# Kernel tuning notes

Hardware: AMD Instinct MI355X
Metric: run time of the kernel (lower is better)

Reference implementation:

```python
import jax, jax.numpy as jnp
import numpy as np

B, S, E, H = 2, 2048, 1024, 16
HD = E // H


def setup_inputs() -> dict:
    key = jax.random.key(0)
    ks = jax.random.split(key, 9)
    s = 1.0 / np.sqrt(E)
    return {
        "x": jax.random.normal(ks[0], (B, S, E), dtype=jnp.float32),
        "wq": jax.random.uniform(ks[1], (E, E), jnp.float32, -s, s),
        "bq": jax.random.uniform(ks[2], (E,), jnp.float32, -s, s),
        "wk": jax.random.uniform(ks[3], (E, E), jnp.float32, -s, s),
        "bk": jax.random.uniform(ks[4], (E,), jnp.float32, -s, s),
        "wv": jax.random.uniform(ks[5], (E, E), jnp.float32, -s, s),
        "bv": jax.random.uniform(ks[6], (E,), jnp.float32, -s, s),
        "wo": jax.random.uniform(ks[7], (E, E), jnp.float32, -s, s),
        "bo": jax.random.uniform(ks[8], (E,), jnp.float32, -s, s),
    }


def reference(x, wq, bq, wk, bk, wv, bv, wo, bo):
    b, s, e = x.shape
    # QKV projections, reshape to [b, h, s, hd]
    def proj(w, bias):
        y = jnp.einsum('bse,ef->bsf', x, w.T) + bias
        return y.reshape(b, s, H, HD).transpose(0, 2, 1, 3)
    q = proj(wq, bq)
    k = proj(wk, bk)
    v = proj(wv, bv)
    score = jnp.einsum('bhqd,bhkd->bhqk', q, k) / jnp.sqrt(jnp.float32(HD))
    # original: exp(x)/sum(exp(x)) + 1e-8  == softmax(x) + 1e-8
    attn = jax.nn.softmax(score, axis=-1) + 1e-8
    out = jnp.einsum('bhqk,bhkd->bhqd', attn, v)
    out = out.transpose(0, 2, 1, 3).reshape(b, s, e)
    return jnp.einsum('bse,ef->bsf', out, wo.T) + bo
```

## Files before the change

kernel.cpp:

```cpp
#include <hip/hip_runtime.h>
#include <hip/hip_bf16.h>
#include <cstdint>

#define SS 2048
#define EE 1024
#define HH 16
#define HDD 64

typedef __attribute__((ext_vector_type(8))) __bf16 bf16x8;
typedef __attribute__((ext_vector_type(4))) float f32x4;

#define MFMA16(a, b, c) __builtin_amdgcn_mfma_f32_16x16x32_bf16((a), (b), (c), 0, 0, 0)

__device__ __forceinline__ unsigned short f2bf(float f) {
    unsigned int u = __builtin_bit_cast(unsigned int, f);
    u += 0x7FFFu + ((u >> 16) & 1u);
    return (unsigned short)(u >> 16);
}

__device__ __forceinline__ float bcf(unsigned int u) {
    return __builtin_bit_cast(float, u);
}

__device__ __forceinline__ void gll16(const unsigned short* g, unsigned short* l) {
    __builtin_amdgcn_global_load_lds(
        (__attribute__((address_space(1))) unsigned int*)g,
        (__attribute__((address_space(3))) unsigned int*)l, 16, 0, 0);
}

__device__ __forceinline__ void pl32swap(unsigned int& a, unsigned int& b) {
#if __has_builtin(__builtin_amdgcn_permlane32_swap)
    auto r = __builtin_amdgcn_permlane32_swap(a, b, false, false);
    a = r[0]; b = r[1];
#else
    unsigned int as = __shfl_xor(a, 32, 64), bs = __shfl_xor(b, 32, 64);
    const bool hi = (threadIdx.x & 32) != 0;
    unsigned int na = hi ? bs : a, nb = hi ? b : as;
    a = na; b = nb;
#endif
}

__device__ __forceinline__ void pl16swap(unsigned int& a, unsigned int& b) {
#if __has_builtin(__builtin_amdgcn_permlane16_swap)
    auto r = __builtin_amdgcn_permlane16_swap(a, b, false, false);
    a = r[0]; b = r[1];
#else
    unsigned int as = __shfl_xor(a, 16, 64), bs = __shfl_xor(b, 16, 64);
    const bool odd = (threadIdx.x & 16) != 0;
    unsigned int na = odd ? bs : a, nb = odd ? b : as;
    a = na; b = nb;
#endif
}

__global__ __launch_bounds__(256) void cvt_all(
    const float* __restrict__ x, const float* __restrict__ wq, const float* __restrict__ wk,
    const float* __restrict__ wv, const float* __restrict__ wo,
    unsigned short* __restrict__ xb, unsigned short* __restrict__ wqb, unsigned short* __restrict__ wkb,
    unsigned short* __restrict__ wvb, unsigned short* __restrict__ wob) {
    int idx = blockIdx.x * 256 + threadIdx.x;
    int i4 = idx << 2;
    const float* src;
    unsigned short* dst;
    int off;
    if (i4 < 4194304) { src = x; dst = xb; off = i4; }
    else {
        int w = (i4 - 4194304) >> 20;
        off = (i4 - 4194304) & 1048575;
        if (w == 0) { src = wq; dst = wqb; }
        else if (w == 1) { src = wk; dst = wkb; }
        else if (w == 2) { src = wv; dst = wvb; }
        else { src = wo; dst = wob; }
    }
    float4 v = *(const float4*)&src[off];
    unsigned int p0 = (unsigned int)f2bf(v.x) | ((unsigned int)f2bf(v.y) << 16);
    unsigned int p1 = (unsigned int)f2bf(v.z) | ((unsigned int)f2bf(v.w) << 16);
    uint2 u; u.x = p0; u.y = p1;
    *(uint2*)&dst[off] = u;
}

template <int MODE, int BMT, int BNT>
__device__ __forceinline__ void gemm_core(
    unsigned short* __restrict__ lsA,
    unsigned short* __restrict__ lsB,
    const unsigned short* __restrict__ A, const unsigned short* __restrict__ W,
    const float* __restrict__ bias, void* __restrict__ out, int bm, int bn) {
    constexpr int IT = BMT / 32, JT = BNT / 32;
    constexpr int ASTR = BMT * 32, BSTR = BNT * 32;
    const int t = threadIdx.x;
    const int lane = t & 63, l15 = lane & 15, quad = lane >> 4;
    const int wave = t >> 6;
    const int wm = (wave >> 1) * (BMT / 2), wn = (wave & 1) * (BNT / 2);

    const int cg = ((t & 3) ^ ((t >> 3) & 3)) * 8;
    const unsigned short* ga = A + (size_t)(bm + (t >> 2)) * 1024 + cg;
    const unsigned short* gb = W + (size_t)(bn + (t >> 2)) * 1024 + cg;

    f32x4 acc[IT][JT];
    for (int i = 0; i < IT; i++)
        for (int j = 0; j < JT; j++) acc[i][j] = (f32x4){0.f, 0.f, 0.f, 0.f};

    const int swz = (l15 >> 1) & 3;

    gll16(ga, &lsA[t * 8]);
    if (BMT == 128) gll16(ga + 64 * 1024, &lsA[2048 + t * 8]);
    gll16(gb, &lsB[t * 8]);
    if (BNT == 128) gll16(gb + 64 * 1024, &lsB[2048 + t * 8]);

    for (int it = 0; it < 32; it++) {
        const int cur = it & 1, nxt = cur ^ 1;
        __syncthreads();

        if (it < 31) {
            const int k0 = (it + 1) * 32;
            gll16(ga + k0, &lsA[nxt * ASTR + t * 8]);
            if (BMT == 128) gll16(ga + k0 + 64 * 1024, &lsA[nxt * ASTR + 2048 + t * 8]);
            gll16(gb + k0, &lsB[nxt * BSTR + t * 8]);
            if (BNT == 128) gll16(gb + k0 + 64 * 1024, &lsB[nxt * BSTR + 2048 + t * 8]);
        }

        bf16x8 af[IT], bfr[JT];
        for (int i = 0; i < IT; i++)
            af[i] = *(const bf16x8*)&lsA[cur * ASTR + (wm + i * 16 + l15) * 32 + ((quad ^ swz) * 8)];
        for (int j = 0; j < JT; j++)
            bfr[j] = *(const bf16x8*)&lsB[cur * BSTR + (wn + j * 16 + l15) * 32 + ((quad ^ swz) * 8)];
        for (int i = 0; i < IT; i++)
            for (int j = 0; j < JT; j++) acc[i][j] = MFMA16(af[i], bfr[j], acc[i][j]);
    }

    for (int j = 0; j < JT; j++) {
        int n = bn + wn + j * 16 + l15;
        float bj = bias[n];
        for (int i = 0; i < IT; i++) {
            int m0 = bm + wm + i * 16 + quad * 4;
            int srow0 = m0 & 2047, bidx = m0 >> 11;
            if (MODE == 3) {
                size_t headb = ((size_t)bidx * HH + (n >> 6)) * (SS * HDD);
                size_t base = headb + (size_t)(srow0 >> 6) * 4096 +
                              (size_t)(((srow0 >> 4) & 3) * 8 + ((n & 63) >> 3)) * 128 + (n & 7);
                for (int rg = 0; rg < 4; rg++)
                    ((unsigned short*)out)[base + (size_t)((srow0 & 15) + rg) * 8] = f2bf(acc[i][j][rg] + bj);
            } else if (MODE == 4) {
                size_t headb = ((size_t)bidx * HH + (n >> 6)) * (SS * HDD);
                size_t addr = headb + (size_t)(srow0 >> 6) * 4096 + (size_t)((n & 63) >> 4) * 1024 +
                              (size_t)(((srow0 >> 5) & 1) * 4 + ((srow0 >> 3) & 3)) * 128 +
                              (size_t)(n & 15) * 8 + (srow0 & 7);
                float v0 = acc[i][j][0] + bj, v1 = acc[i][j][1] + bj;
                float v2 = acc[i][j][2] + bj, v3 = acc[i][j][3] + bj;
                uint2 w;
                w.x = (unsigned int)f2bf(v0) | ((unsigned int)f2bf(v1) << 16);
                w.y = (unsigned int)f2bf(v2) | ((unsigned int)f2bf(v3) << 16);
                *(uint2*)&((unsigned short*)out)[addr] = w;
            } else {
                for (int rg = 0; rg < 4; rg++) {
                    float val = acc[i][j][rg] + bj;
                    int m = m0 + rg;
                    if (MODE == 0) {
                        ((unsigned short*)out)[(((size_t)(m >> 11) * HH + (n >> 6)) * SS + (m & 2047)) * HDD + (n & 63)] = f2bf(val);
                    } else {
                        ((float*)out)[(size_t)m * 1024 + n] = val;
                    }
                }
            }
        }
    }
}

__global__ __launch_bounds__(256) void gemm_qkv(
    const unsigned short* __restrict__ xb,
    const unsigned short* __restrict__ wqb, const unsigned short* __restrict__ wkb,
    const unsigned short* __restrict__ wvb,
    const float* __restrict__ bq, const float* __restrict__ bk, const float* __restrict__ bv,
    unsigned short* qb, unsigned short* kb, unsigned short* vtb) {
    __shared__ unsigned short shA[2 * 4096];
    __shared__ unsigned short shB[2 * 4096];
    const int blk = blockIdx.x;
    const int u = blk & 7, r = blk >> 3;
    const int by = u + 8 * (r & 3);
    const int rest = r >> 2;
    const int bx = rest & 7, z = rest >> 3;
    if (z == 0)      gemm_core<0, 128, 128>(shA, shB, xb, wqb, bq, qb,  by * 128, bx * 128);
    else if (z == 1) gemm_core<3, 128, 128>(shA, shB, xb, wkb, bk, kb,  by * 128, bx * 128);
    else             gemm_core<4, 128, 128>(shA, shB, xb, wvb, bv, vtb, by * 128, bx * 128);
}

__global__ __launch_bounds__(256) void gemm_out(
    const unsigned short* __restrict__ ob, const unsigned short* __restrict__ wob,
    const float* __restrict__ bo, float* __restrict__ out) {
    __shared__ unsigned short shA[2 * 4096];
    __shared__ unsigned short shB[2 * 2048];
    const int blk = blockIdx.x;
    const int u = blk & 7, r = blk >> 3;
    const int by = u + 8 * (r & 3);
    const int bx = r >> 2;
    gemm_core<1, 128, 64>(shA, shB, ob, wob, bo, out, by * 128, bx * 64);
}

__global__ __launch_bounds__(512, 4) void attn_fwd(
    const unsigned short* __restrict__ qb, const unsigned short* __restrict__ kb,
    const unsigned short* __restrict__ vtb, unsigned short* __restrict__ ob) {
    __shared__ unsigned short sh[20480];
    unsigned short* lsK = sh;
    unsigned short* lsV = sh + 8192;
    const int t = threadIdx.x, lane = t & 63, l15 = lane & 15, quad = lane >> 4;
    const int wave = t >> 6;
    const int half = wave >> 2;
    const int wq = wave & 3;
    const int tg = t & 255;
    const int blk = blockIdx.x;
    const int u = blk & 7, r = blk >> 3;
    const int bh = u + 8 * (r & 3);
    const int qt = r >> 2;
    const size_t hoff = (size_t)bh * (SS * HDD);
    const float C = 0.125f * 1.44269504088896f;

    bf16x8 qf[2][2];
    const int qrow = qt * 128 + wq * 32;
    for (int i = 0; i < 2; i++)
        for (int ks = 0; ks < 2; ks++) {
            bf16x8 raw = *(const bf16x8*)&qb[hoff + (size_t)(qrow + i * 16 + l15) * HDD + ks * 32 + quad * 8];
            unsigned short tmp[8];
            *(bf16x8*)tmp = raw;
            for (int j = 0; j < 8; j++) {
                float f = __builtin_bit_cast(float, (unsigned int)tmp[j] << 16);
                tmp[j] = f2bf(f * C);
            }
            qf[i][ks] = *(const bf16x8*)tmp;
        }

    f32x4 o[2][4];
    float ps[2] = {0.f, 0.f};
    for (int i = 0; i < 2; i++)
        for (int jh = 0; jh < 4; jh++) o[i][jh] = (f32x4){0.f, 0.f, 0.f, 0.f};

    const unsigned short* gk = kb + hoff + (size_t)half * 16 * 4096;
    const unsigned short* gv = vtb + hoff + (size_t)half * 16 * 4096;
    unsigned short* myK = lsK + half * 4096;
    unsigned short* myV = lsV + half * 4096;
    const int foff = quad * 128 + l15 * 8;

    gll16(gk + tg * 8, myK + tg * 8);
    gll16(gk + 2048 + tg * 8, myK + 2048 + tg * 8);
    gll16(gv + tg * 8, myV + tg * 8);
    gll16(gv + 2048 + tg * 8, myV + 2048 + tg * 8);

    for (int kt = 0; kt < 16; kt++) {
        __syncthreads();

        bf16x8 kfr[4][2];
        for (int j = 0; j < 4; j++)
            for (int ks = 0; ks < 2; ks++)
                kfr[j][ks] = *(const bf16x8*)&myK[j * 1024 + ks * 512 + foff];

        f32x4 st[2][4];
        for (int j = 0; j < 4; j++)
            for (int i = 0; i < 2; i++) {
                f32x4 z = (f32x4){0.f, 0.f, 0.f, 0.f};
                z = MFMA16(kfr[j][0], qf[i][0], z);
                z = MFMA16(kfr[j][1], qf[i][1], z);
                st[i][j] = z;
            }

        bf16x8 pf[2][2];
        for (int i = 0; i < 2; i++) {
            unsigned int W[4][2];
            float accp = 0.f;
            for (int j = 0; j < 4; j++) {
                float e0 = __builtin_amdgcn_exp2f(st[i][j][0]);
                float e1 = __builtin_amdgcn_exp2f(st[i][j][1]);
                float e2 = __builtin_amdgcn_exp2f(st[i][j][2]);
                float e3 = __builtin_amdgcn_exp2f(st[i][j][3]);
                unsigned int w0 = (__builtin_bit_cast(unsigned int, e0) >> 16) |
                                  (__builtin_bit_cast(unsigned int, e1) & 0xFFFF0000u);
                unsigned int w1 = (__builtin_bit_cast(unsigned int, e2) >> 16) |
                                  (__builtin_bit_cast(unsigned int, e3) & 0xFFFF0000u);
                W[j][0] = w0; W[j][1] = w1;
                accp += (bcf(w0 << 16) + bcf(w0 & 0xFFFF0000u)) +
                        (bcf(w1 << 16) + bcf(w1 & 0xFFFF0000u));
            }
            ps[i] += accp;

            unsigned int P0[4], P1[4];
            for (int h = 0; h < 2; h++) {
                unsigned int x = W[0][h], y = W[1][h];
                pl32swap(x, y);
                pl16swap(x, y);
                P0[h] = x; P0[2 + h] = y;
                unsigned int x2 = W[2][h], y2 = W[3][h];
                pl32swap(x2, y2);
                pl16swap(x2, y2);
                P1[h] = x2; P1[2 + h] = y2;
            }
            union { unsigned int u4[4]; bf16x8 v; } cv0, cv1;
            for (int p = 0; p < 4; p++) { cv0.u4[p] = P0[p]; cv1.u4[p] = P1[p]; }
            pf[i][0] = cv0.v;
            pf[i][1] = cv1.v;
        }

        for (int jh = 0; jh < 4; jh++) {
            bf16x8 v0 = *(const bf16x8*)&myV[jh * 1024 + foff];
            bf16x8 v1 = *(const bf16x8*)&myV[jh * 1024 + 512 + foff];
            for (int i = 0; i < 2; i++) {
                o[i][jh] = MFMA16(pf[i][0], v0, o[i][jh]);
                o[i][jh] = MFMA16(pf[i][1], v1, o[i][jh]);
            }
        }

        if (kt < 15) {
            __syncthreads();
            const unsigned short* gkn = gk + (kt + 1) * 4096;
            const unsigned short* gvn = gv + (kt + 1) * 4096;
            gll16(gkn + tg * 8, myK + tg * 8);
            gll16(gkn + 2048 + tg * 8, myK + 2048 + tg * 8);
            gll16(gvn + tg * 8, myV + tg * 8);
            gll16(gvn + 2048 + tg * 8, myV + 2048 + tg * 8);
        }
    }

    float mysum[2][4];
    for (int i = 0; i < 2; i++) {
        float xv = ps[i];
        xv += __shfl_xor(xv, 16, 64);
        xv += __shfl_xor(xv, 32, 64);
        for (int rg = 0; rg < 4; rg++)
            mysum[i][rg] = __shfl(xv, quad * 20 + rg, 64);
    }

    __syncthreads();
    float* cb = (float*)sh;
    float* lb = cb + 8192;
    const int lslot = wq * 64 + lane;
    if (half == 1) {
        for (int i = 0; i < 2; i++)
            for (int jh = 0; jh < 4; jh++)
                for (int rg = 0; rg < 4; rg++)
                    cb[(i * 16 + jh * 4 + rg) * 256 + lslot] = o[i][jh][rg];
        for (int i = 0; i < 2; i++)
            for (int rg = 0; rg < 4; rg++)
                lb[(i * 4 + rg) * 256 + lslot] = mysum[i][rg];
    }
    __syncthreads();
    if (half == 0) {
        const int b = bh >> 4, h = bh & 15;
        for (int i = 0; i < 2; i++)
            for (int rg = 0; rg < 4; rg++) {
                float inv = 1.f / (mysum[i][rg] + lb[(i * 4 + rg) * 256 + lslot]);
                int srow = qrow + i * 16 + quad * 4 + rg;
                size_t rowoff = ((size_t)b * SS + srow) * EE + h * 64;
                for (int jh = 0; jh < 4; jh++) {
                    float val = o[i][jh][rg] + cb[(i * 16 + jh * 4 + rg) * 256 + lslot];
                    ob[rowoff + jh * 16 + l15] = f2bf(val * inv);
                }
            }
    }
}

extern "C" void kernel_launch(void* const* d_in, const int* in_sizes, int n_in,
                              void* d_out, int out_size, void* d_ws, size_t ws_size,
                              hipStream_t stream) {
    const float* x  = (const float*)d_in[0];
    const float* wq = (const float*)d_in[1];
    const float* bq = (const float*)d_in[2];
    const float* wk = (const float*)d_in[3];
    const float* bk = (const float*)d_in[4];
    const float* wv = (const float*)d_in[5];
    const float* bv = (const float*)d_in[6];
    const float* wo = (const float*)d_in[7];
    const float* bo = (const float*)d_in[8];

    char* ws = (char*)d_ws;
    unsigned short* xb  = (unsigned short*)(ws + 0);
    unsigned short* wqb = (unsigned short*)(ws + 8388608);
    unsigned short* wkb = (unsigned short*)(ws + 10485760);
    unsigned short* wvb = (unsigned short*)(ws + 12582912);
    unsigned short* wob = (unsigned short*)(ws + 14680064);
    unsigned short* qb  = (unsigned short*)(ws + 16777216);
    unsigned short* kb  = (unsigned short*)(ws + 25165824);
    unsigned short* vtb = (unsigned short*)(ws + 33554432);
    unsigned short* ob  = xb;

    cvt_all<<<8192, 256, 0, stream>>>(x, wq, wk, wv, wo, xb, wqb, wkb, wvb, wob);
    gemm_qkv<<<768, 256, 0, stream>>>(xb, wqb, wkb, wvb, bq, bk, bv, qb, kb, vtb);
    attn_fwd<<<512, 512, 0, stream>>>(qb, kb, vtb, ob);
    gemm_out<<<512, 256, 0, stream>>>(ob, wob, bo, (float*)d_out);
}
```

Before: 189.6 us.

## Double-buffer K/V tiles in attention and compute row sums with MFMA

Doubles the LDS K/V staging buffers so the next tile is loaded asynchronously while the current one is computed, which removes the second barrier per iteration. The per-row softmax denominator is now accumulated by running an MFMA of P against a ones vector instead of unpacking bf16 values and summing with scalar adds and shuffles. The cost is twice the LDS per block, which may reduce occupancy, plus two extra MFMAs per row block per tile.

```diff
diff --git a/kernel.cpp b/kernel.cpp
--- a/kernel.cpp
+++ b/kernel.cpp
@@ -16,10 +16,6 @@
     unsigned int u = __builtin_bit_cast(unsigned int, f);
     u += 0x7FFFu + ((u >> 16) & 1u);
     return (unsigned short)(u >> 16);
-}
-
-__device__ __forceinline__ float bcf(unsigned int u) {
-    return __builtin_bit_cast(float, u);
 }
 
 __device__ __forceinline__ void gll16(const unsigned short* g, unsigned short* l) {
@@ -198,9 +194,9 @@
 __global__ __launch_bounds__(512, 4) void attn_fwd(
     const unsigned short* __restrict__ qb, const unsigned short* __restrict__ kb,
     const unsigned short* __restrict__ vtb, unsigned short* __restrict__ ob) {
-    __shared__ unsigned short sh[20480];
+    __shared__ unsigned short sh[32768];
     unsigned short* lsK = sh;
-    unsigned short* lsV = sh + 8192;
+    unsigned short* lsV = sh + 16384;
     const int t = threadIdx.x, lane = t & 63, l15 = lane & 15, quad = lane >> 4;
     const int wave = t >> 6;
     const int half = wave >> 2;
@@ -227,24 +223,42 @@
             qf[i][ks] = *(const bf16x8*)tmp;
         }
 
+    unsigned short onesbuf[8];
+    for (int j = 0; j < 8; j++) onesbuf[j] = 0x3F80;
+    const bf16x8 onesf = *(const bf16x8*)onesbuf;
+
+    f32x4 lacc[2];
     f32x4 o[2][4];
-    float ps[2] = {0.f, 0.f};
-    for (int i = 0; i < 2; i++)
+    for (int i = 0; i < 2; i++) {
+        lacc[i] = (f32x4){0.f, 0.f, 0.f, 0.f};
         for (int jh = 0; jh < 4; jh++) o[i][jh] = (f32x4){0.f, 0.f, 0.f, 0.f};
+    }
 
     const unsigned short* gk = kb + hoff + (size_t)half * 16 * 4096;
     const unsigned short* gv = vtb + hoff + (size_t)half * 16 * 4096;
-    unsigned short* myK = lsK + half * 4096;
-    unsigned short* myV = lsV + half * 4096;
     const int foff = quad * 128 + l15 * 8;
 
-    gll16(gk + tg * 8, myK + tg * 8);
-    gll16(gk + 2048 + tg * 8, myK + 2048 + tg * 8);
-    gll16(gv + tg * 8, myV + tg * 8);
-    gll16(gv + 2048 + tg * 8, myV + 2048 + tg * 8);
+    auto stage = [&](int buf, int tile) {
+        unsigned short* dk = lsK + buf * 8192 + half * 4096;
+        unsigned short* dv = lsV + buf * 8192 + half * 4096;
+        const unsigned short* sk = gk + tile * 4096;
+        const unsigned short* sv = gv + tile * 4096;
+        gll16(sk + tg * 8, dk + tg * 8);
+        gll16(sk + 2048 + tg * 8, dk + 2048 + tg * 8);
+        gll16(sv + tg * 8, dv + tg * 8);
+        gll16(sv + 2048 + tg * 8, dv + 2048 + tg * 8);
+    };
+
+    stage(0, 0);
 
     for (int kt = 0; kt < 16; kt++) {
+        const int cur = kt & 1;
         __syncthreads();
+
+        if (kt < 15) stage(cur ^ 1, kt + 1);
+
+        const unsigned short* myK = lsK + cur * 8192 + half * 4096;
+        const unsigned short* myV = lsV + cur * 8192 + half * 4096;
 
         bf16x8 kfr[4][2];
         for (int j = 0; j < 4; j++)
@@ -263,21 +277,16 @@
         bf16x8 pf[2][2];
         for (int i = 0; i < 2; i++) {
             unsigned int W[4][2];
-            float accp = 0.f;
             for (int j = 0; j < 4; j++) {
                 float e0 = __builtin_amdgcn_exp2f(st[i][j][0]);
                 float e1 = __builtin_amdgcn_exp2f(st[i][j][1]);
                 float e2 = __builtin_amdgcn_exp2f(st[i][j][2]);
                 float e3 = __builtin_amdgcn_exp2f(st[i][j][3]);
-                unsigned int w0 = (__builtin_bit_cast(unsigned int, e0) >> 16) |
-                                  (__builtin_bit_cast(unsigned int, e1) & 0xFFFF0000u);
-                unsigned int w1 = (__builtin_bit_cast(unsigned int, e2) >> 16) |
-                                  (__builtin_bit_cast(unsigned int, e3) & 0xFFFF0000u);
-                W[j][0] = w0; W[j][1] = w1;
-                accp += (bcf(w0 << 16) + bcf(w0 & 0xFFFF0000u)) +
-                        (bcf(w1 << 16) + bcf(w1 & 0xFFFF0000u));
-            }
-            ps[i] += accp;
+                W[j][0] = (__builtin_bit_cast(unsigned int, e0) >> 16) |
+                          (__builtin_bit_cast(unsigned int, e1) & 0xFFFF0000u);
+                W[j][1] = (__builtin_bit_cast(unsigned int, e2) >> 16) |
+                          (__builtin_bit_cast(unsigned int, e3) & 0xFFFF0000u);
+            }
 
             unsigned int P0[4], P1[4];
             for (int h = 0; h < 2; h++) {
@@ -304,25 +313,10 @@
                 o[i][jh] = MFMA16(pf[i][1], v1, o[i][jh]);
             }
         }
-
-        if (kt < 15) {
-            __syncthreads();
-            const unsigned short* gkn = gk + (kt + 1) * 4096;
-            const unsigned short* gvn = gv + (kt + 1) * 4096;
-            gll16(gkn + tg * 8, myK + tg * 8);
-            gll16(gkn + 2048 + tg * 8, myK + 2048 + tg * 8);
-            gll16(gvn + tg * 8, myV + tg * 8);
-            gll16(gvn + 2048 + tg * 8, myV + 2048 + tg * 8);
-        }
-    }
-
-    float mysum[2][4];
-    for (int i = 0; i < 2; i++) {
-        float xv = ps[i];
-        xv += __shfl_xor(xv, 16, 64);
-        xv += __shfl_xor(xv, 32, 64);
-        for (int rg = 0; rg < 4; rg++)
-            mysum[i][rg] = __shfl(xv, quad * 20 + rg, 64);
+        for (int i = 0; i < 2; i++) {
+            lacc[i] = MFMA16(pf[i][0], onesf, lacc[i]);
+            lacc[i] = MFMA16(pf[i][1], onesf, lacc[i]);
+        }
     }
 
     __syncthreads();
@@ -336,14 +330,14 @@
                     cb[(i * 16 + jh * 4 + rg) * 256 + lslot] = o[i][jh][rg];
         for (int i = 0; i < 2; i++)
             for (int rg = 0; rg < 4; rg++)
-                lb[(i * 4 + rg) * 256 + lslot] = mysum[i][rg];
+                lb[(i * 4 + rg) * 256 + lslot] = lacc[i][rg];
     }
     __syncthreads();
     if (half == 0) {
         const int b = bh >> 4, h = bh & 15;
         for (int i = 0; i < 2; i++)
             for (int rg = 0; rg < 4; rg++) {
-                float inv = 1.f / (mysum[i][rg] + lb[(i * 4 + rg) * 256 + lslot]);
+                float inv = 1.f / (lacc[i][rg] + lb[(i * 4 + rg) * 256 + lslot]);
                 int srow = qrow + i * 16 + quad * 4 + rg;
                 size_t rowoff = ((size_t)b * SS + srow) * EE + h * 64;
                 for (int jh = 0; jh < 4; jh++) {
```

Measured after the change: 187.8 us. About the same (-0.9%).
